# Kernel tuning notes

Measured on AMD Instinct MI355X. Metric: run time of the kernel, lower is better.

Reference implementation:

```python
import jax, jax.numpy as jnp
import numpy as np

N_V = 100000
N_E = 20000
NNZ = 1600000
D = 128


def setup_inputs() -> dict:
    key = jax.random.key(0)
    k1, k2, k3, k4, k5 = jax.random.split(key, 5)
    X = jax.random.normal(k1, (N_V, D), dtype=jnp.float32)
    W = jax.random.normal(k2, (D, D), dtype=jnp.float32) * (1.0 / np.sqrt(D))
    b = jax.random.normal(k3, (D,), dtype=jnp.float32) * 0.01
    v2e_src = jax.random.randint(k4, (NNZ,), 0, N_V, dtype=jnp.int32)
    v2e_dst = jax.random.randint(k5, (NNZ,), 0, N_E, dtype=jnp.int32)
    return {"X": X, "W": W, "b": b, "v2e_src": v2e_src, "v2e_dst": v2e_dst, "num_e": N_E}


def reference(X, W, b, v2e_src, v2e_dst, num_e):
    num_v = X.shape[0]
    ones = jnp.ones(v2e_src.shape[0], dtype=X.dtype)
    # node degrees (values of D_v diagonal) and hyperedge incidence counts
    deg_v = jax.ops.segment_sum(ones, v2e_src, num_segments=num_v)
    cnt_e = jax.ops.segment_sum(ones, v2e_dst, num_segments=num_e)

    # theta: linear layer
    Xt = X @ W.T + b  # [N_V, D]

    # v2e mean aggregation: per hyperedge, mean of incident vertex features
    Ysum = jax.ops.segment_sum(Xt[v2e_src], v2e_dst, num_segments=num_e)  # [N_E, D]
    Y = Ysum / jnp.maximum(cnt_e, 1.0)[:, None]

    # edge norm: torch scatter_reduce(reduce='mean', include_self=True) -> sum/(count+1)
    De_sum = jax.ops.segment_sum(deg_v[v2e_src], v2e_dst, num_segments=num_e)
    De = De_sum / (cnt_e + 1.0)
    De = jnp.where(De > 0, jax.lax.rsqrt(jnp.maximum(De, 1e-30)), 1.0)  # inf -> 1
    Y = De[:, None] * Y

    # e2v sum aggregation
    Xo = jax.ops.segment_sum(Y[v2e_dst], v2e_src, num_segments=num_v)  # [N_V, D]

    # D_v^{-1/2} sparse diagonal mm (zero-degree nodes -> 0)
    dvn = jnp.where(deg_v > 0, jax.lax.rsqrt(jnp.maximum(deg_v, 1e-30)), 0.0)
    Xo = dvn[:, None] * Xo

    # is_last=False: ReLU then dropout (dropout is identity in eval)
    return jax.nn.relu(Xo)
```

## Files before the change

kernel.cpp:

```cpp
#include <hip/hip_runtime.h>
#include <hip/hip_bf16.h>

#define NV 100000
#define NE 20000
#define DD 128
#define ESHIFT 7
#define VSHIFT 9
#define NBE 157
#define NBV 196
#define NBK 256
#define CHUNK 4096
#define CAPE 11264
#define CAPV 9216

using bf16 = __hip_bfloat16;

typedef __attribute__((ext_vector_type(8))) short frag_ab;
typedef __attribute__((ext_vector_type(4))) float frag_cd;

__device__ __forceinline__ float uas(unsigned u) { union { unsigned u; float f; } c; c.u = u; return c.f; }
__device__ __forceinline__ unsigned pk2(float lo, float hi) {
    bf16 l = __float2bfloat16(lo), h = __float2bfloat16(hi);
    return (unsigned)(*(unsigned short*)&l) | ((unsigned)(*(unsigned short*)&h) << 16);
}
__device__ __forceinline__ void accum8(float* a, uint4 x) {
    a[0] += uas(x.x << 16); a[1] += uas(x.x & 0xffff0000u);
    a[2] += uas(x.y << 16); a[3] += uas(x.y & 0xffff0000u);
    a[4] += uas(x.z << 16); a[5] += uas(x.z & 0xffff0000u);
    a[6] += uas(x.w << 16); a[7] += uas(x.w & 0xffff0000u);
}

__global__ void init_cur(int* __restrict__ bcur_e, int* __restrict__ bcur_v) {
    int t = threadIdx.x;
    bcur_e[t] = t * CAPE;
    bcur_v[t] = t * CAPV;
}

__global__ __launch_bounds__(256) void partition_and_cvt(const int* __restrict__ src, const int* __restrict__ dst,
                                                         int* __restrict__ bcur_e, int* __restrict__ bcur_v,
                                                         unsigned* __restrict__ pairs_e, unsigned* __restrict__ pairs_v,
                                                         int nnz,
                                                         const float4* __restrict__ Xf, ushort4* __restrict__ Xb,
                                                         const float4* __restrict__ Wf, ushort4* __restrict__ Wb) {
    int nchunk = (nnz + CHUNK - 1) / CHUNK;
    int t = threadIdx.x;
    if ((int)blockIdx.x >= nchunk) {
        const int n4x = NV * DD / 4;
        const int n4w = DD * DD / 4;
        int i = ((int)blockIdx.x - nchunk) * 256 + t;
        if (i < n4x + n4w) {
            float4 v;
            ushort4 o;
            if (i < n4x) v = Xf[i]; else v = Wf[i - n4x];
            bf16 a = __float2bfloat16(v.x); o.x = *(unsigned short*)&a;
            bf16 b = __float2bfloat16(v.y); o.y = *(unsigned short*)&b;
            bf16 c = __float2bfloat16(v.z); o.z = *(unsigned short*)&c;
            bf16 d = __float2bfloat16(v.w); o.w = *(unsigned short*)&d;
            if (i < n4x) Xb[i] = o; else Wb[i - n4x] = o;
        }
        return;
    }
    __shared__ int cnt[NBK], sc[NBK], loff[NBK], gbase[NBK];
    __shared__ unsigned stage[CHUNK];
    int base = blockIdx.x * CHUNK;
    unsigned p[16];
    int rk[16];
#pragma unroll
    for (int k = 0; k < 16; ++k) {
        int i = base + k * 256 + t;
        p[k] = (i < nnz) ? (((unsigned)src[i] << 15) | (unsigned)dst[i]) : 0xFFFFFFFFu;
    }

    cnt[t] = 0;
    __syncthreads();
#pragma unroll
    for (int k = 0; k < 16; ++k)
        if (p[k] != 0xFFFFFFFFu) rk[k] = atomicAdd(&cnt[(p[k] >> ESHIFT) & 0xFF], 1);
    __syncthreads();
    sc[t] = cnt[t];
    __syncthreads();
    for (int o = 1; o < NBK; o <<= 1) { int x = (t >= o) ? sc[t - o] : 0; __syncthreads(); sc[t] += x; __syncthreads(); }
    loff[t] = sc[t] - cnt[t];
    gbase[t] = (cnt[t] > 0) ? atomicAdd(&bcur_e[t], cnt[t]) : 0;
    __syncthreads();
#pragma unroll
    for (int k = 0; k < 16; ++k)
        if (p[k] != 0xFFFFFFFFu) stage[loff[(p[k] >> ESHIFT) & 0xFF] + rk[k]] = p[k];
    __syncthreads();
    {
        int wid = t >> 6, ln = t & 63;
        for (int b2 = wid; b2 < NBK; b2 += 4) {
            int n = cnt[b2], lo = loff[b2], gb = gbase[b2];
            for (int idx = ln; idx < n; idx += 64) pairs_e[gb + idx] = stage[lo + idx];
        }
    }
    __syncthreads();

    cnt[t] = 0;
    __syncthreads();
#pragma unroll
    for (int k = 0; k < 16; ++k)
        if (p[k] != 0xFFFFFFFFu) rk[k] = atomicAdd(&cnt[p[k] >> 24], 1);
    __syncthreads();
    sc[t] = cnt[t];
    __syncthreads();
    for (int o = 1; o < NBK; o <<= 1) { int x = (t >= o) ? sc[t - o] : 0; __syncthreads(); sc[t] += x; __syncthreads(); }
    loff[t] = sc[t] - cnt[t];
    gbase[t] = (cnt[t] > 0) ? atomicAdd(&bcur_v[t], cnt[t]) : 0;
    __syncthreads();
#pragma unroll
    for (int k = 0; k < 16; ++k)
        if (p[k] != 0xFFFFFFFFu) stage[loff[p[k] >> 24] + rk[k]] = p[k];
    __syncthreads();
    {
        int wid = t >> 6, ln = t & 63;
        for (int b2 = wid; b2 < NBK; b2 += 4) {
            int n = cnt[b2], lo = loff[b2], gb = gbase[b2];
            for (int idx = ln; idx < n; idx += 64) pairs_v[gb + idx] = stage[lo + idx];
        }
    }
}

__global__ __launch_bounds__(1024) void build_csr(const unsigned* __restrict__ pairs_e, const int* __restrict__ bcur_e,
                                                  int* __restrict__ off_e, int* __restrict__ end_e, int* __restrict__ e_src,
                                                  const unsigned* __restrict__ pairs_v, const int* __restrict__ bcur_v,
                                                  int* __restrict__ off_v, int* __restrict__ end_v, int* __restrict__ v_edge,
                                                  int* __restrict__ deg_v) {
    __shared__ int cnt[512], sc2[512], cur[512];
    int t = threadIdx.x;
    if ((int)blockIdx.x < NBE) {
        int b = blockIdx.x;
        int lo = b * CAPE, hi = bcur_e[b];
        if (t < 128) cnt[t] = 0;
        __syncthreads();
        for (int i = lo + t; i < hi; i += 1024) atomicAdd(&cnt[pairs_e[i] & 127], 1);
        __syncthreads();
        if (t < 128) sc2[t] = cnt[t];
        __syncthreads();
        for (int o = 1; o < 128; o <<= 1) {
            int x = 0;
            if (t < 128 && t >= o) x = sc2[t - o];
            __syncthreads();
            if (t < 128) sc2[t] += x;
            __syncthreads();
        }
        if (t < 128) {
            int ex = sc2[t] - cnt[t];
            cur[t] = ex;
            int e = (b << ESHIFT) + t;
            if (e < NE) { off_e[e] = lo + ex; end_e[e] = lo + ex + cnt[t]; }
        }
        __syncthreads();
        for (int i = lo + t; i < hi; i += 1024) {
            unsigned p = pairs_e[i];
            int r = atomicAdd(&cur[p & 127], 1);
            e_src[lo + r] = (int)(p >> 15);
        }
    } else {
        int b = blockIdx.x - NBE;
        int lo = b * CAPV, hi = bcur_v[b];
        if (t < 512) cnt[t] = 0;
        __syncthreads();
        for (int i = lo + t; i < hi; i += 1024) atomicAdd(&cnt[(pairs_v[i] >> 15) & 511], 1);
        __syncthreads();
        if (t < 512) sc2[t] = cnt[t];
        __syncthreads();
        for (int o = 1; o < 512; o <<= 1) {
            int x = 0;
            if (t < 512 && t >= o) x = sc2[t - o];
            __syncthreads();
            if (t < 512) sc2[t] += x;
            __syncthreads();
        }
        if (t < 512) {
            int ex = sc2[t] - cnt[t];
            cur[t] = ex;
            int v = (b << VSHIFT) + t;
            if (v < NV) { off_v[v] = lo + ex; end_v[v] = lo + ex + cnt[t]; deg_v[v] = cnt[t]; }
        }
        __syncthreads();
        for (int i = lo + t; i < hi; i += 1024) {
            unsigned p = pairs_v[i];
            int r = atomicAdd(&cur[(p >> 15) & 511], 1);
            v_edge[lo + r] = (int)(p & 0x7FFF);
        }
    }
}

__global__ __launch_bounds__(256) void edge_agg(const uint4* __restrict__ Xq, const int* __restrict__ off_e,
                                                const int* __restrict__ end_e,
                                                const int* __restrict__ e_src, const int* __restrict__ deg_v,
                                                uint4* __restrict__ Sq, float* __restrict__ beta) {
    int wave = (blockIdx.x * blockDim.x + threadIdx.x) >> 6;
    int lane = threadIdx.x & 63;
    if (wave >= NE) return;
    int g = lane >> 4, l16 = lane & 15;
    int start = off_e[wave], end = end_e[wave];
    float acc[8] = {0.f, 0.f, 0.f, 0.f, 0.f, 0.f, 0.f, 0.f};
    float degsum = 0.f;
    int j = start;
    for (; j + 16 <= end; j += 16) {
        int s0 = e_src[j + g];
        int s1 = e_src[j + 4 + g];
        int s2 = e_src[j + 8 + g];
        int s3 = e_src[j + 12 + g];
        uint4 x0 = Xq[(size_t)s0 * 16 + l16];
        uint4 x1 = Xq[(size_t)s1 * 16 + l16];
        uint4 x2 = Xq[(size_t)s2 * 16 + l16];
        uint4 x3 = Xq[(size_t)s3 * 16 + l16];
        degsum += (float)(deg_v[s0] + deg_v[s1] + deg_v[s2] + deg_v[s3]);
        accum8(acc, x0);
        accum8(acc, x1);
        accum8(acc, x2);
        accum8(acc, x3);
    }
    for (; j < end; j += 4) {
        int idx = j + g;
        if (idx < end) {
            int s = e_src[idx];
            uint4 x = Xq[(size_t)s * 16 + l16];
            degsum += (float)deg_v[s];
            accum8(acc, x);
        }
    }
#pragma unroll
    for (int i = 0; i < 8; ++i) {
        acc[i] += __shfl_xor(acc[i], 16);
        acc[i] += __shfl_xor(acc[i], 32);
    }
    degsum += __shfl_xor(degsum, 16);
    degsum += __shfl_xor(degsum, 32);

    float cntf = (float)(end - start);
    float Des = degsum / (cntf + 1.0f);
    float De = (Des > 0.f) ? rsqrtf(fmaxf(Des, 1e-30f)) : 1.0f;
    float scale = De / fmaxf(cntf, 1.0f);
    if (g == 0) {
        uint4 o;
        o.x = pk2(acc[0] * scale, acc[1] * scale);
        o.y = pk2(acc[2] * scale, acc[3] * scale);
        o.z = pk2(acc[4] * scale, acc[5] * scale);
        o.w = pk2(acc[6] * scale, acc[7] * scale);
        Sq[(size_t)wave * 16 + l16] = o;
        if (l16 == 0) beta[wave] = (cntf > 0.f) ? De : 0.f;
    }
}

__global__ __launch_bounds__(256) void gemm_edge(const bf16* __restrict__ S, const bf16* __restrict__ Wb,
                                                 const float* __restrict__ bias, const float* __restrict__ beta,
                                                 bf16* __restrict__ Y) {
    int wave = (blockIdx.x * blockDim.x + threadIdx.x) >> 6;
    int lane = threadIdx.x & 63;
    int mBase = wave * 16;
    if (mBase >= NE) return;
    int l16 = lane & 15, quad = lane >> 4;

    const short* Ss = (const short*)S;
    const short* Ws = (const short*)Wb;

    frag_ab a[4];
#pragma unroll
    for (int kt = 0; kt < 4; ++kt)
        a[kt] = *(const frag_ab*)(Ss + (size_t)(mBase + l16) * DD + kt * 32 + quad * 8);

    float beta_r[4];
#pragma unroll
    for (int r = 0; r < 4; ++r) beta_r[r] = beta[mBase + quad * 4 + r];

#pragma unroll
    for (int nt = 0; nt < 8; ++nt) {
        frag_cd acc = {0.f, 0.f, 0.f, 0.f};
#pragma unroll
        for (int kt = 0; kt < 4; ++kt) {
            frag_ab bfr = *(const frag_ab*)(Ws + (size_t)(nt * 16 + l16) * DD + kt * 32 + quad * 8);
            acc = __builtin_amdgcn_mfma_f32_16x16x32_bf16(a[kt], bfr, acc, 0, 0, 0);
        }
        float bv = bias[nt * 16 + l16];
#pragma unroll
        for (int r = 0; r < 4; ++r) {
            int row = mBase + quad * 4 + r;
            float v = acc[r] + beta_r[r] * bv;
            Y[(size_t)row * DD + nt * 16 + l16] = __float2bfloat16(v);
        }
    }
}

__global__ __launch_bounds__(256) void vertex_agg(const uint4* __restrict__ Yq, const int* __restrict__ off_v,
                                                  const int* __restrict__ end_v,
                                                  const int* __restrict__ v_edge, float* __restrict__ out) {
    int wave = (blockIdx.x * blockDim.x + threadIdx.x) >> 6;
    int lane = threadIdx.x & 63;
    if (wave >= NV) return;
    int g = lane >> 4, l16 = lane & 15;
    int start = off_v[wave], end = end_v[wave];
    float acc[8] = {0.f, 0.f, 0.f, 0.f, 0.f, 0.f, 0.f, 0.f};
    int j = start;
    for (; j + 8 <= end; j += 8) {
        int e0 = v_edge[j + g];
        int e1 = v_edge[j + 4 + g];
        uint4 y0 = Yq[(size_t)e0 * 16 + l16];
        uint4 y1 = Yq[(size_t)e1 * 16 + l16];
        accum8(acc, y0);
        accum8(acc, y1);
    }
    for (; j < end; j += 4) {
        int idx = j + g;
        if (idx < end) {
            int e = v_edge[idx];
            uint4 y = Yq[(size_t)e * 16 + l16];
            accum8(acc, y);
        }
    }
#pragma unroll
    for (int i = 0; i < 8; ++i) {
        acc[i] += __shfl_xor(acc[i], 16);
        acc[i] += __shfl_xor(acc[i], 32);
    }
    int deg = end - start;
    float dvn = (deg > 0) ? rsqrtf((float)deg) : 0.f;
    if (g == 0) {
        float4 o1, o2;
        o1.x = fmaxf(acc[0] * dvn, 0.f);
        o1.y = fmaxf(acc[1] * dvn, 0.f);
        o1.z = fmaxf(acc[2] * dvn, 0.f);
        o1.w = fmaxf(acc[3] * dvn, 0.f);
        o2.x = fmaxf(acc[4] * dvn, 0.f);
        o2.y = fmaxf(acc[5] * dvn, 0.f);
        o2.z = fmaxf(acc[6] * dvn, 0.f);
        o2.w = fmaxf(acc[7] * dvn, 0.f);
        float4* op = (float4*)(out + (size_t)wave * DD + l16 * 8);
        op[0] = o1;
        op[1] = o2;
    }
}

extern "C" void kernel_launch(void* const* d_in, const int* in_sizes, int n_in,
                              void* d_out, int out_size, void* d_ws, size_t ws_size,
                              hipStream_t stream) {
    const float* X = (const float*)d_in[0];
    const float* W = (const float*)d_in[1];
    const float* b = (const float*)d_in[2];
    const int* src = (const int*)d_in[3];
    const int* dst = (const int*)d_in[4];
    int nnz = in_sizes[3];

    char* ws = (char*)d_ws;
    size_t o = 0;
    auto take = [&](size_t bytes) -> char* {
        char* p = ws + o;
        o += (bytes + 255) & ~(size_t)255;
        return p;
    };
    int* bcur_e = (int*)take(NBK * 4);
    int* bcur_v = (int*)take(NBK * 4);
    int* off_e = (int*)take((size_t)NE * 4);
    int* end_e = (int*)take((size_t)NE * 4);
    int* off_v = (int*)take((size_t)NV * 4);
    int* end_v = (int*)take((size_t)NV * 4);
    int* deg_v = (int*)take((size_t)NV * 4);
    int* e_src = (int*)take((size_t)NBE * CAPE * 4);
    int* v_edge = (int*)take((size_t)NBV * CAPV * 4);
    unsigned* pairs_e = (unsigned*)take((size_t)NBE * CAPE * 4);
    unsigned* pairs_v = (unsigned*)take((size_t)NBV * CAPV * 4);
    float* beta = (float*)take((size_t)NE * 4);
    bf16* S = (bf16*)take((size_t)NE * DD * 2);
    bf16* Y = (bf16*)take((size_t)NE * DD * 2);
    bf16* Wb = (bf16*)take((size_t)DD * DD * 2);
    bf16* Xb = (bf16*)take((size_t)NV * DD * 2);
    (void)ws_size; (void)n_in; (void)out_size;

    int nchunk = (nnz + CHUNK - 1) / CHUNK;
    int ncvt = (NV * DD / 4 + DD * DD / 4 + 255) / 256;

    init_cur<<<1, NBK, 0, stream>>>(bcur_e, bcur_v);
    partition_and_cvt<<<nchunk + ncvt, 256, 0, stream>>>(src, dst, bcur_e, bcur_v, pairs_e, pairs_v, nnz,
                                                         (const float4*)X, (ushort4*)Xb,
                                                         (const float4*)W, (ushort4*)Wb);
    build_csr<<<NBE + NBV, 1024, 0, stream>>>(pairs_e, bcur_e, off_e, end_e, e_src,
                                              pairs_v, bcur_v, off_v, end_v, v_edge, deg_v);

    edge_agg<<<NE * 64 / 256, 256, 0, stream>>>((const uint4*)Xb, off_e, end_e, e_src, deg_v, (uint4*)S, beta);
    gemm_edge<<<(NE / 16 * 64 + 255) / 256, 256, 0, stream>>>(S, Wb, b, beta, Y);
    vertex_agg<<<NV * 64 / 256, 256, 0, stream>>>((const uint4*)Y, off_v, end_v, v_edge, (float*)d_out);
}
```

Before: 277.1 us.

## Fuse edge aggregation with GEMM and split shared-memory histograms to cut contention

Merges edge_agg and gemm_edge into a single kernel: each block aggregates 16 hyperedges into an LDS tile and then runs the MFMA projection from LDS, so the S and beta buffers no longer go through global memory. The partition and CSR-build kernels now use per-subgroup histograms to reduce LDS atomic contention, and build_csr keeps pairs and ranks in registers instead of re-reading them for a second atomic pass. vertex_agg unrolls its gather loop to 16 neighbours per iteration. The fused kernel has fewer waves per hyperedge (4 edges per wave, serial), which lowers parallelism in the gather phase.

```diff
diff --git a/kernel.cpp b/kernel.cpp
--- a/kernel.cpp
+++ b/kernel.cpp
@@ -60,8 +60,9 @@
         }
         return;
     }
-    __shared__ int cnt[NBK], sc[NBK], loff[NBK], gbase[NBK];
+    __shared__ int cntA[NBK], cntB[NBK], pre1[NBK], tot[NBK], sc[NBK], loff[NBK], gbase[NBK];
     __shared__ unsigned stage[CHUNK];
+    int sub = t >> 7;
     int base = blockIdx.x * CHUNK;
     unsigned p[16];
     int rk[16];
@@ -71,51 +72,69 @@
         p[k] = (i < nnz) ? (((unsigned)src[i] << 15) | (unsigned)dst[i]) : 0xFFFFFFFFu;
     }
 
-    cnt[t] = 0;
+    cntA[t] = 0; cntB[t] = 0;
     __syncthreads();
 #pragma unroll
     for (int k = 0; k < 16; ++k)
-        if (p[k] != 0xFFFFFFFFu) rk[k] = atomicAdd(&cnt[(p[k] >> ESHIFT) & 0xFF], 1);
-    __syncthreads();
-    sc[t] = cnt[t];
+        if (p[k] != 0xFFFFFFFFu) {
+            int b = (p[k] >> ESHIFT) & 0xFF;
+            rk[k] = atomicAdd(sub ? &cntB[b] : &cntA[b], 1);
+        }
+    __syncthreads();
+    {
+        int a = cntA[t], b = cntB[t];
+        pre1[t] = a; tot[t] = a + b; sc[t] = a + b;
+    }
     __syncthreads();
     for (int o = 1; o < NBK; o <<= 1) { int x = (t >= o) ? sc[t - o] : 0; __syncthreads(); sc[t] += x; __syncthreads(); }
-    loff[t] = sc[t] - cnt[t];
-    gbase[t] = (cnt[t] > 0) ? atomicAdd(&bcur_e[t], cnt[t]) : 0;
+    loff[t] = sc[t] - tot[t];
+    gbase[t] = (tot[t] > 0) ? atomicAdd(&bcur_e[t], tot[t]) : 0;
     __syncthreads();
 #pragma unroll
     for (int k = 0; k < 16; ++k)
-        if (p[k] != 0xFFFFFFFFu) stage[loff[(p[k] >> ESHIFT) & 0xFF] + rk[k]] = p[k];
+        if (p[k] != 0xFFFFFFFFu) {
+            int b = (p[k] >> ESHIFT) & 0xFF;
+            stage[loff[b] + rk[k] + (sub ? pre1[b] : 0)] = p[k];
+        }
     __syncthreads();
     {
         int wid = t >> 6, ln = t & 63;
         for (int b2 = wid; b2 < NBK; b2 += 4) {
-            int n = cnt[b2], lo = loff[b2], gb = gbase[b2];
+            int n = tot[b2], lo = loff[b2], gb = gbase[b2];
             for (int idx = ln; idx < n; idx += 64) pairs_e[gb + idx] = stage[lo + idx];
         }
     }
     __syncthreads();
 
-    cnt[t] = 0;
+    cntA[t] = 0; cntB[t] = 0;
     __syncthreads();
 #pragma unroll
     for (int k = 0; k < 16; ++k)
-        if (p[k] != 0xFFFFFFFFu) rk[k] = atomicAdd(&cnt[p[k] >> 24], 1);
-    __syncthreads();
-    sc[t] = cnt[t];
+        if (p[k] != 0xFFFFFFFFu) {
+            int b = p[k] >> 24;
+            rk[k] = atomicAdd(sub ? &cntB[b] : &cntA[b], 1);
+        }
+    __syncthreads();
+    {
+        int a = cntA[t], b = cntB[t];
+        pre1[t] = a; tot[t] = a + b; sc[t] = a + b;
+    }
     __syncthreads();
     for (int o = 1; o < NBK; o <<= 1) { int x = (t >= o) ? sc[t - o] : 0; __syncthreads(); sc[t] += x; __syncthreads(); }
-    loff[t] = sc[t] - cnt[t];
-    gbase[t] = (cnt[t] > 0) ? atomicAdd(&bcur_v[t], cnt[t]) : 0;
+    loff[t] = sc[t] - tot[t];
+    gbase[t] = (tot[t] > 0) ? atomicAdd(&bcur_v[t], tot[t]) : 0;
     __syncthreads();
 #pragma unroll
     for (int k = 0; k < 16; ++k)
-        if (p[k] != 0xFFFFFFFFu) stage[loff[p[k] >> 24] + rk[k]] = p[k];
+        if (p[k] != 0xFFFFFFFFu) {
+            int b = p[k] >> 24;
+            stage[loff[b] + rk[k] + (sub ? pre1[b] : 0)] = p[k];
+        }
     __syncthreads();
     {
         int wid = t >> 6, ln = t & 63;
         for (int b2 = wid; b2 < NBK; b2 += 4) {
-            int n = cnt[b2], lo = loff[b2], gb = gbase[b2];
+            int n = tot[b2], lo = loff[b2], gb = gbase[b2];
             for (int idx = ln; idx < n; idx += 64) pairs_v[gb + idx] = stage[lo + idx];
         }
     }
@@ -126,16 +145,29 @@
                                                   const unsigned* __restrict__ pairs_v, const int* __restrict__ bcur_v,
                                                   int* __restrict__ off_v, int* __restrict__ end_v, int* __restrict__ v_edge,
                                                   int* __restrict__ deg_v) {
-    __shared__ int cnt[512], sc2[512], cur[512];
+    __shared__ int cA[2048], cB[2048], sc2[512], eoff[512];
     int t = threadIdx.x;
+    cA[t] = 0; cA[t + 1024] = 0;
+    __syncthreads();
     if ((int)blockIdx.x < NBE) {
         int b = blockIdx.x;
         int lo = b * CAPE, hi = bcur_e[b];
-        if (t < 128) cnt[t] = 0;
-        __syncthreads();
-        for (int i = lo + t; i < hi; i += 1024) atomicAdd(&cnt[pairs_e[i] & 127], 1);
-        __syncthreads();
-        if (t < 128) sc2[t] = cnt[t];
+        int sub = t >> 7;
+        unsigned pv[12];
+        int rk[12];
+        int kk = 0;
+        for (int i = lo + t; i < hi; i += 1024, ++kk) {
+            unsigned p = pairs_e[i];
+            pv[kk] = p;
+            rk[kk] = atomicAdd(&cA[sub * 128 + (p & 127)], 1);
+        }
+        __syncthreads();
+        if (t < 128) {
+            int run = 0;
+#pragma unroll
+            for (int s = 0; s < 8; ++s) { cB[s * 128 + t] = run; run += cA[s * 128 + t]; }
+            sc2[t] = run;
+        }
         __syncthreads();
         for (int o = 1; o < 128; o <<= 1) {
             int x = 0;
@@ -145,25 +177,37 @@
             __syncthreads();
         }
         if (t < 128) {
-            int ex = sc2[t] - cnt[t];
-            cur[t] = ex;
+            int totalb = cB[7 * 128 + t] + cA[7 * 128 + t];
+            int ex = sc2[t] - totalb;
+            eoff[t] = ex;
             int e = (b << ESHIFT) + t;
-            if (e < NE) { off_e[e] = lo + ex; end_e[e] = lo + ex + cnt[t]; }
-        }
-        __syncthreads();
-        for (int i = lo + t; i < hi; i += 1024) {
-            unsigned p = pairs_e[i];
-            int r = atomicAdd(&cur[p & 127], 1);
-            e_src[lo + r] = (int)(p >> 15);
+            if (e < NE) { off_e[e] = lo + ex; end_e[e] = lo + ex + totalb; }
+        }
+        __syncthreads();
+        for (int k = 0; k < kk; ++k) {
+            int bkt = pv[k] & 127;
+            int pos = lo + eoff[bkt] + cB[sub * 128 + bkt] + rk[k];
+            e_src[pos] = (int)(pv[k] >> 15);
         }
     } else {
         int b = blockIdx.x - NBE;
         int lo = b * CAPV, hi = bcur_v[b];
-        if (t < 512) cnt[t] = 0;
-        __syncthreads();
-        for (int i = lo + t; i < hi; i += 1024) atomicAdd(&cnt[(pairs_v[i] >> 15) & 511], 1);
-        __syncthreads();
-        if (t < 512) sc2[t] = cnt[t];
+        int sub = t >> 8;
+        unsigned pv[9];
+        int rk[9];
+        int kk = 0;
+        for (int i = lo + t; i < hi; i += 1024, ++kk) {
+            unsigned p = pairs_v[i];
+            pv[kk] = p;
+            rk[kk] = atomicAdd(&cA[sub * 512 + ((p >> 15) & 511)], 1);
+        }
+        __syncthreads();
+        if (t < 512) {
+            int run = 0;
+#pragma unroll
+            for (int s = 0; s < 4; ++s) { cB[s * 512 + t] = run; run += cA[s * 512 + t]; }
+            sc2[t] = run;
+        }
         __syncthreads();
         for (int o = 1; o < 512; o <<= 1) {
             int x = 0;
@@ -173,102 +217,101 @@
             __syncthreads();
         }
         if (t < 512) {
-            int ex = sc2[t] - cnt[t];
-            cur[t] = ex;
+            int totalb = cB[3 * 512 + t] + cA[3 * 512 + t];
+            int ex = sc2[t] - totalb;
+            eoff[t] = ex;
             int v = (b << VSHIFT) + t;
-            if (v < NV) { off_v[v] = lo + ex; end_v[v] = lo + ex + cnt[t]; deg_v[v] = cnt[t]; }
-        }
-        __syncthreads();
-        for (int i = lo + t; i < hi; i += 1024) {
-            unsigned p = pairs_v[i];
-            int r = atomicAdd(&cur[(p >> 15) & 511], 1);
-            v_edge[lo + r] = (int)(p & 0x7FFF);
-        }
-    }
-}
-
-__global__ __launch_bounds__(256) void edge_agg(const uint4* __restrict__ Xq, const int* __restrict__ off_e,
-                                                const int* __restrict__ end_e,
-                                                const int* __restrict__ e_src, const int* __restrict__ deg_v,
-                                                uint4* __restrict__ Sq, float* __restrict__ beta) {
-    int wave = (blockIdx.x * blockDim.x + threadIdx.x) >> 6;
-    int lane = threadIdx.x & 63;
-    if (wave >= NE) return;
+            if (v < NV) { off_v[v] = lo + ex; end_v[v] = lo + ex + totalb; deg_v[v] = totalb; }
+        }
+        __syncthreads();
+        for (int k = 0; k < kk; ++k) {
+            int bkt = (pv[k] >> 15) & 511;
+            int pos = lo + eoff[bkt] + cB[sub * 512 + bkt] + rk[k];
+            v_edge[pos] = (int)(pv[k] & 0x7FFF);
+        }
+    }
+}
+
+__global__ __launch_bounds__(256) void edge_fused(const uint4* __restrict__ Xq, const int* __restrict__ off_e,
+                                                  const int* __restrict__ end_e,
+                                                  const int* __restrict__ e_src, const int* __restrict__ deg_v,
+                                                  const bf16* __restrict__ Wb, const float* __restrict__ bias,
+                                                  bf16* __restrict__ Y) {
+    __shared__ short Stile[16][136];
+    __shared__ float betaL[16];
+    int t = threadIdx.x;
+    int w = t >> 6, lane = t & 63;
     int g = lane >> 4, l16 = lane & 15;
-    int start = off_e[wave], end = end_e[wave];
-    float acc[8] = {0.f, 0.f, 0.f, 0.f, 0.f, 0.f, 0.f, 0.f};
-    float degsum = 0.f;
-    int j = start;
-    for (; j + 16 <= end; j += 16) {
-        int s0 = e_src[j + g];
-        int s1 = e_src[j + 4 + g];
-        int s2 = e_src[j + 8 + g];
-        int s3 = e_src[j + 12 + g];
-        uint4 x0 = Xq[(size_t)s0 * 16 + l16];
-        uint4 x1 = Xq[(size_t)s1 * 16 + l16];
-        uint4 x2 = Xq[(size_t)s2 * 16 + l16];
-        uint4 x3 = Xq[(size_t)s3 * 16 + l16];
-        degsum += (float)(deg_v[s0] + deg_v[s1] + deg_v[s2] + deg_v[s3]);
-        accum8(acc, x0);
-        accum8(acc, x1);
-        accum8(acc, x2);
-        accum8(acc, x3);
-    }
-    for (; j < end; j += 4) {
-        int idx = j + g;
-        if (idx < end) {
-            int s = e_src[idx];
-            uint4 x = Xq[(size_t)s * 16 + l16];
-            degsum += (float)deg_v[s];
-            accum8(acc, x);
-        }
-    }
-#pragma unroll
-    for (int i = 0; i < 8; ++i) {
-        acc[i] += __shfl_xor(acc[i], 16);
-        acc[i] += __shfl_xor(acc[i], 32);
-    }
-    degsum += __shfl_xor(degsum, 16);
-    degsum += __shfl_xor(degsum, 32);
-
-    float cntf = (float)(end - start);
-    float Des = degsum / (cntf + 1.0f);
-    float De = (Des > 0.f) ? rsqrtf(fmaxf(Des, 1e-30f)) : 1.0f;
-    float scale = De / fmaxf(cntf, 1.0f);
-    if (g == 0) {
-        uint4 o;
-        o.x = pk2(acc[0] * scale, acc[1] * scale);
-        o.y = pk2(acc[2] * scale, acc[3] * scale);
-        o.z = pk2(acc[4] * scale, acc[5] * scale);
-        o.w = pk2(acc[6] * scale, acc[7] * scale);
-        Sq[(size_t)wave * 16 + l16] = o;
-        if (l16 == 0) beta[wave] = (cntf > 0.f) ? De : 0.f;
-    }
-}
-
-__global__ __launch_bounds__(256) void gemm_edge(const bf16* __restrict__ S, const bf16* __restrict__ Wb,
-                                                 const float* __restrict__ bias, const float* __restrict__ beta,
-                                                 bf16* __restrict__ Y) {
-    int wave = (blockIdx.x * blockDim.x + threadIdx.x) >> 6;
-    int lane = threadIdx.x & 63;
-    int mBase = wave * 16;
-    if (mBase >= NE) return;
-    int l16 = lane & 15, quad = lane >> 4;
-
-    const short* Ss = (const short*)S;
+    int mBase = blockIdx.x * 16;
+
+    for (int ei = 0; ei < 4; ++ei) {
+        int le = w * 4 + ei;
+        int e = mBase + le;
+        int start = off_e[e], end = end_e[e];
+        float acc[8] = {0.f, 0.f, 0.f, 0.f, 0.f, 0.f, 0.f, 0.f};
+        float degsum = 0.f;
+        int j = start;
+        for (; j + 16 <= end; j += 16) {
+            int s0 = e_src[j + g];
+            int s1 = e_src[j + 4 + g];
+            int s2 = e_src[j + 8 + g];
+            int s3 = e_src[j + 12 + g];
+            uint4 x0 = Xq[(size_t)s0 * 16 + l16];
+            uint4 x1 = Xq[(size_t)s1 * 16 + l16];
+            uint4 x2 = Xq[(size_t)s2 * 16 + l16];
+            uint4 x3 = Xq[(size_t)s3 * 16 + l16];
+            degsum += (float)(deg_v[s0] + deg_v[s1] + deg_v[s2] + deg_v[s3]);
+            accum8(acc, x0);
+            accum8(acc, x1);
+            accum8(acc, x2);
+            accum8(acc, x3);
+        }
+        for (; j < end; j += 4) {
+            int idx = j + g;
+            if (idx < end) {
+                int s = e_src[idx];
+                uint4 x = Xq[(size_t)s * 16 + l16];
+                degsum += (float)deg_v[s];
+                accum8(acc, x);
+            }
+        }
+#pragma unroll
+        for (int i = 0; i < 8; ++i) {
+            acc[i] += __shfl_xor(acc[i], 16);
+            acc[i] += __shfl_xor(acc[i], 32);
+        }
+        degsum += __shfl_xor(degsum, 16);
+        degsum += __shfl_xor(degsum, 32);
+
+        float cntf = (float)(end - start);
+        float Des = degsum / (cntf + 1.0f);
+        float De = (Des > 0.f) ? rsqrtf(fmaxf(Des, 1e-30f)) : 1.0f;
+        float scale = De / fmaxf(cntf, 1.0f);
+        if (g == 0) {
+            uint4 o;
+            o.x = pk2(acc[0] * scale, acc[1] * scale);
+            o.y = pk2(acc[2] * scale, acc[3] * scale);
+            o.z = pk2(acc[4] * scale, acc[5] * scale);
+            o.w = pk2(acc[6] * scale, acc[7] * scale);
+            *(uint4*)&Stile[le][l16 * 8] = o;
+            if (l16 == 0) betaL[le] = (cntf > 0.f) ? De : 0.f;
+        }
+    }
+    __syncthreads();
+
     const short* Ws = (const short*)Wb;
-
+    int quad = g;
     frag_ab a[4];
 #pragma unroll
     for (int kt = 0; kt < 4; ++kt)
-        a[kt] = *(const frag_ab*)(Ss + (size_t)(mBase + l16) * DD + kt * 32 + quad * 8);
-
+        a[kt] = *(const frag_ab*)&Stile[l16][kt * 32 + quad * 8];
     float beta_r[4];
 #pragma unroll
-    for (int r = 0; r < 4; ++r) beta_r[r] = beta[mBase + quad * 4 + r];
-
-#pragma unroll
-    for (int nt = 0; nt < 8; ++nt) {
+    for (int r = 0; r < 4; ++r) beta_r[r] = betaL[quad * 4 + r];
+
+#pragma unroll
+    for (int nn = 0; nn < 2; ++nn) {
+        int nt = w * 2 + nn;
         frag_cd acc = {0.f, 0.f, 0.f, 0.f};
 #pragma unroll
         for (int kt = 0; kt < 4; ++kt) {
@@ -295,13 +338,19 @@
     int start = off_v[wave], end = end_v[wave];
     float acc[8] = {0.f, 0.f, 0.f, 0.f, 0.f, 0.f, 0.f, 0.f};
     int j = start;
-    for (; j + 8 <= end; j += 8) {
+    for (; j + 16 <= end; j += 16) {
         int e0 = v_edge[j + g];
         int e1 = v_edge[j + 4 + g];
+        int e2 = v_edge[j + 8 + g];
+        int e3 = v_edge[j + 12 + g];
         uint4 y0 = Yq[(size_t)e0 * 16 + l16];
         uint4 y1 = Yq[(size_t)e1 * 16 + l16];
+        uint4 y2 = Yq[(size_t)e2 * 16 + l16];
+        uint4 y3 = Yq[(size_t)e3 * 16 + l16];
         accum8(acc, y0);
         accum8(acc, y1);
+        accum8(acc, y2);
+        accum8(acc, y3);
     }
     for (; j < end; j += 4) {
         int idx = j + g;
@@ -362,8 +411,6 @@
     int* v_edge = (int*)take((size_t)NBV * CAPV * 4);
     unsigned* pairs_e = (unsigned*)take((size_t)NBE * CAPE * 4);
     unsigned* pairs_v = (unsigned*)take((size_t)NBV * CAPV * 4);
-    float* beta = (float*)take((size_t)NE * 4);
-    bf16* S = (bf16*)take((size_t)NE * DD * 2);
     bf16* Y = (bf16*)take((size_t)NE * DD * 2);
     bf16* Wb = (bf16*)take((size_t)DD * DD * 2);
     bf16* Xb = (bf16*)take((size_t)NV * DD * 2);
@@ -378,8 +425,6 @@
                                                          (const float4*)W, (ushort4*)Wb);
     build_csr<<<NBE + NBV, 1024, 0, stream>>>(pairs_e, bcur_e, off_e, end_e, e_src,
                                               pairs_v, bcur_v, off_v, end_v, v_edge, deg_v);
-
-    edge_agg<<<NE * 64 / 256, 256, 0, stream>>>((const uint4*)Xb, off_e, end_e, e_src, deg_v, (uint4*)S, beta);
-    gemm_edge<<<(NE / 16 * 64 + 255) / 256, 256, 0, stream>>>(S, Wb, b, beta, Y);
+    edge_fused<<<NE / 16, 256, 0, stream>>>((const uint4*)Xb, off_e, end_e, e_src, deg_v, Wb, b, Y);
     vertex_agg<<<NV * 64 / 256, 256, 0, stream>>>((const uint4*)Y, off_v, end_v, v_edge, (float*)d_out);
 }
```

After: 268.0 us. 1.03x faster.
